# Optimization experiments

Hardware: AMD Instinct MI355X
Metric: run time of the kernel (lower is better)

Reference implementation:

```python
import jax, jax.numpy as jnp
import numpy as np

CHUNK = 256  # rows of z processed per scan step; keeps [CHUNK, M, D] intermediate ~64MB


def setup_inputs() -> dict:
    key = jax.random.key(0)
    k1, k2, k3, k4 = jax.random.split(key, 4)
    N, M, D = 2048, 512, 128
    z = jax.random.normal(k1, (N, D), dtype=jnp.float32)
    e = jax.random.normal(k2, (M, D), dtype=jnp.float32)
    probs = jax.random.uniform(k3, (N,), dtype=jnp.float32)
    dropout = jax.random.uniform(k4, (N, D), dtype=jnp.float32)
    return {"z": z, "e": e, "probs": probs, "dropout": dropout}


def reference(z, e, probs, dropout):
    # z: [N, D], e: [M, D]
    N, D = z.shape
    M = e.shape[0]
    nchunk = N // CHUNK

    def body(carry, zc):
        # zc: [CHUNK, D]
        min_sum, min_elem = carry  # [M], [M, D]
        # elementwise squared differences for this chunk: [CHUNK, M, D]
        delem = (zc[:, None, :] - e[None, :, :]) ** 2
        dsum = jnp.sum(delem, axis=2)                      # [CHUNK, M]
        min_sum = jnp.minimum(min_sum, jnp.min(dsum, axis=0))
        min_elem = jnp.minimum(min_elem, jnp.min(delem, axis=0))
        return (min_sum, min_elem), None

    init = (jnp.full((M,), jnp.inf, dtype=z.dtype),
            jnp.full((M, D), jnp.inf, dtype=z.dtype))
    (min_sum, min_elem), _ = jax.lax.scan(body, init, z.reshape(nchunk, CHUNK, D))

    # torch: mean over M of min over N of sum_d distance
    min_loss = jnp.mean(min_sum)
    # torch: mean over (M, D) of elementwise min over N
    wise_min_loss = jnp.mean(min_elem)

    # z = z * (dropout < probs[:, None])  -- boolean mask multiply
    z_out = z * (dropout < probs[:, None]).astype(z.dtype)
    return min_loss, wise_min_loss, z_out
```

## Files before the change

### kernel.cpp

```cpp
#include <hip/hip_runtime.h>


#define N_ 2048
#define M_ 512
#define D_ 128
#define ME_OFF  M_
#define CNT_OFF (M_ + M_ * D_)
#define POISON  0xAAAAAAAAu
#define CONTRIB 768u

__global__ void __launch_bounds__(256, 2) k_all(
        const float* __restrict__ z, const float* __restrict__ e,
        const float* __restrict__ probs, const float* __restrict__ drop,
        float* __restrict__ out, unsigned int* __restrict__ ws) {
    const int bx = blockIdx.x;
    const int t  = threadIdx.x;
    bool contrib = true;

    if (bx < 512) {
        const int mg = bx >> 3, chunk = bx & 7;
        const int d = t & 127, half = t >> 7;
        const int m0 = mg * 8 + half * 4;
        const int n0 = chunk * 256;

        const float e0 = e[(m0 + 0) * D_ + d];
        const float e1 = e[(m0 + 1) * D_ + d];
        const float e2 = e[(m0 + 2) * D_ + d];
        const float e3 = e[(m0 + 3) * D_ + d];

        float me0 = __uint_as_float(0x7f800000u), me1 = me0, me2 = me0, me3 = me0;
        const float* zp = z + n0 * D_ + d;
        #pragma unroll 8
        for (int i = 0; i < 256; ++i) {
            float zv = zp[i * D_];
            float df;
            df = zv - e0; me0 = fminf(me0, df * df);
            df = zv - e1; me1 = fminf(me1, df * df);
            df = zv - e2; me2 = fminf(me2, df * df);
            df = zv - e3; me3 = fminf(me3, df * df);
        }
        unsigned int* me = ws + ME_OFF + m0 * D_ + d;
        atomicMin(me + 0 * D_, __float_as_uint(me0));
        atomicMin(me + 1 * D_, __float_as_uint(me1));
        atomicMin(me + 2 * D_, __float_as_uint(me2));
        atomicMin(me + 3 * D_, __float_as_uint(me3));
    } else if (bx < 768) {
        const int b = bx - 512;
        const int nb = b >> 5, mt = b & 31;
        const int n = nb * 256 + t;
        const int m0 = mt * 16;

        float4 zr[32];
        const float4* z4 = reinterpret_cast<const float4*>(z) + n * 32;
        #pragma unroll
        for (int j = 0; j < 32; ++j) zr[j] = z4[j];

        const float4* e4 = reinterpret_cast<const float4*>(e);
        for (int mi = 0; mi < 16; mi += 2) {
            const int ma = m0 + mi;
            const int mb = ma + 1;
            float a0 = 0.f, a1 = 0.f, a2 = 0.f, a3 = 0.f;
            float b0 = 0.f, b1 = 0.f, b2 = 0.f, b3 = 0.f;
            #pragma unroll
            for (int j = 0; j < 32; ++j) {
                float4 ea = e4[ma * 32 + j];
                float4 eb = e4[mb * 32 + j];
                float dx, dy, dz, dw;
                dx = zr[j].x - ea.x; a0 = fmaf(dx, dx, a0);
                dy = zr[j].y - ea.y; a1 = fmaf(dy, dy, a1);
                dz = zr[j].z - ea.z; a2 = fmaf(dz, dz, a2);
                dw = zr[j].w - ea.w; a3 = fmaf(dw, dw, a3);
                dx = zr[j].x - eb.x; b0 = fmaf(dx, dx, b0);
                dy = zr[j].y - eb.y; b1 = fmaf(dy, dy, b1);
                dz = zr[j].z - eb.z; b2 = fmaf(dz, dz, b2);
                dw = zr[j].w - eb.w; b3 = fmaf(dw, dw, b3);
            }
            float sa = (a0 + a1) + (a2 + a3);
            float sb = (b0 + b1) + (b2 + b3);
            #pragma unroll
            for (int off = 32; off; off >>= 1) {
                sa = fminf(sa, __shfl_xor(sa, off));
                sb = fminf(sb, __shfl_xor(sb, off));
            }
            if ((t & 63) == 0) {
                atomicMin(&ws[ma], __float_as_uint(sa));
                atomicMin(&ws[mb], __float_as_uint(sb));
            }
        }
    } else {
        contrib = false;
        const int b = bx - 768;
        const int i = b * 256 + t;
        const int n = i >> 5;
        const float p = probs[n];
        const float4 zv = reinterpret_cast<const float4*>(z)[i];
        const float4 dv = reinterpret_cast<const float4*>(drop)[i];
        float2 lo, hi;
        lo.x = dv.x < p ? zv.x : 0.f;
        lo.y = dv.y < p ? zv.y : 0.f;
        hi.x = dv.z < p ? zv.z : 0.f;
        hi.y = dv.w < p ? zv.w : 0.f;
        float2* o = reinterpret_cast<float2*>(out + 2) + i * 2;
        o[0] = lo;
        o[1] = hi;
    }

    if (!contrib) return;

    __shared__ unsigned int lastFlag;
    __syncthreads();
    if (t == 0) {
        __threadfence();
        unsigned int old = atomicAdd(ws + CNT_OFF, 1u);
        lastFlag = (old == POISON + (CONTRIB - 1u)) | (old == CONTRIB - 1u);
    }
    __syncthreads();
    if (!lastFlag) return;

    __threadfence();
    const float* wf = reinterpret_cast<const float*>(ws);

    float s_elem = 0.f;
    const float4* me4 = reinterpret_cast<const float4*>(wf + ME_OFF);
    #pragma unroll 8
    for (int k = 0; k < 64; ++k) {
        float4 v = me4[k * 256 + t];
        s_elem += (v.x + v.y) + (v.z + v.w);
    }
    float s_sum = 0.f;
    if (t < 128) {
        float4 u = reinterpret_cast<const float4*>(wf)[t];
        s_sum = (u.x + u.y) + (u.z + u.w);
    }
    #pragma unroll
    for (int off = 32; off; off >>= 1) {
        s_elem += __shfl_xor(s_elem, off);
        s_sum  += __shfl_xor(s_sum, off);
    }
    __shared__ float sm[8];
    const int w = t >> 6;
    if ((t & 63) == 0) { sm[w] = s_elem; sm[4 + w] = s_sum; }
    __syncthreads();
    if (t == 0) {
        float te = sm[0] + sm[1] + sm[2] + sm[3];
        float ts = sm[4] + sm[5] + sm[6] + sm[7];
        out[0] = ts * (1.0f / 512.0f);
        out[1] = te * (1.0f / 65536.0f);
    }
}

extern "C" void kernel_launch(void* const* d_in, const int* in_sizes, int n_in,
                              void* d_out, int out_size, void* d_ws, size_t ws_size,
                              hipStream_t stream) {
    const float* z     = (const float*)d_in[0];
    const float* e     = (const float*)d_in[1];
    const float* probs = (const float*)d_in[2];
    const float* drop  = (const float*)d_in[3];
    float* out = (float*)d_out;
    unsigned int* ws = (unsigned int*)d_ws;

    k_all<<<dim3(1024), dim3(256), 0, stream>>>(z, e, probs, drop, out, ws);
}
```

Measured before the change: 100.1 us.

## Restructure distance-sum blocks to stream z and keep sixteen accumulators

The sum-distance branch no longer holds a whole z row (32 float4) in registers. It streams z one float4 at a time and updates 16 running sums, one per codebook row, so each z load is reused across 16 rows and the shuffle reductions and atomics are batched. Launch bounds are raised to 4 blocks per SM and the elementwise-min loop unroll is doubled. This lowers register pressure to raise occupancy, at the cost of a single serial FMA chain per accumulator and more e loads per z element.

```diff
diff --git a/kernel.cpp b/kernel.cpp
--- a/kernel.cpp
+++ b/kernel.cpp
@@ -9,7 +9,7 @@
 #define POISON  0xAAAAAAAAu
 #define CONTRIB 768u
 
-__global__ void __launch_bounds__(256, 2) k_all(
+__global__ void __launch_bounds__(256, 4) k_all(
         const float* __restrict__ z, const float* __restrict__ e,
         const float* __restrict__ probs, const float* __restrict__ drop,
         float* __restrict__ out, unsigned int* __restrict__ ws) {
@@ -30,7 +30,7 @@
 
         float me0 = __uint_as_float(0x7f800000u), me1 = me0, me2 = me0, me3 = me0;
         const float* zp = z + n0 * D_ + d;
-        #pragma unroll 8
+        #pragma unroll 16
         for (int i = 0; i < 256; ++i) {
             float zv = zp[i * D_];
             float df;
@@ -50,42 +50,35 @@
         const int n = nb * 256 + t;
         const int m0 = mt * 16;
 
-        float4 zr[32];
+        float s[16];
+        #pragma unroll
+        for (int k = 0; k < 16; ++k) s[k] = 0.f;
+
         const float4* z4 = reinterpret_cast<const float4*>(z) + n * 32;
+        const float4* e4 = reinterpret_cast<const float4*>(e) + m0 * 32;
+
+        #pragma unroll 4
+        for (int j = 0; j < 32; ++j) {
+            const float4 zv = z4[j];
+            #pragma unroll
+            for (int k = 0; k < 16; ++k) {
+                const float4 ev = e4[k * 32 + j];
+                float dx = zv.x - ev.x; s[k] = fmaf(dx, dx, s[k]);
+                float dy = zv.y - ev.y; s[k] = fmaf(dy, dy, s[k]);
+                float dz = zv.z - ev.z; s[k] = fmaf(dz, dz, s[k]);
+                float dw = zv.w - ev.w; s[k] = fmaf(dw, dw, s[k]);
+            }
+        }
         #pragma unroll
-        for (int j = 0; j < 32; ++j) zr[j] = z4[j];
-
-        const float4* e4 = reinterpret_cast<const float4*>(e);
-        for (int mi = 0; mi < 16; mi += 2) {
-            const int ma = m0 + mi;
-            const int mb = ma + 1;
-            float a0 = 0.f, a1 = 0.f, a2 = 0.f, a3 = 0.f;
-            float b0 = 0.f, b1 = 0.f, b2 = 0.f, b3 = 0.f;
+        for (int off = 32; off; off >>= 1) {
             #pragma unroll
-            for (int j = 0; j < 32; ++j) {
-                float4 ea = e4[ma * 32 + j];
-                float4 eb = e4[mb * 32 + j];
-                float dx, dy, dz, dw;
-                dx = zr[j].x - ea.x; a0 = fmaf(dx, dx, a0);
-                dy = zr[j].y - ea.y; a1 = fmaf(dy, dy, a1);
-                dz = zr[j].z - ea.z; a2 = fmaf(dz, dz, a2);
-                dw = zr[j].w - ea.w; a3 = fmaf(dw, dw, a3);
-                dx = zr[j].x - eb.x; b0 = fmaf(dx, dx, b0);
-                dy = zr[j].y - eb.y; b1 = fmaf(dy, dy, b1);
-                dz = zr[j].z - eb.z; b2 = fmaf(dz, dz, b2);
-                dw = zr[j].w - eb.w; b3 = fmaf(dw, dw, b3);
-            }
-            float sa = (a0 + a1) + (a2 + a3);
-            float sb = (b0 + b1) + (b2 + b3);
+            for (int k = 0; k < 16; ++k)
+                s[k] = fminf(s[k], __shfl_xor(s[k], off));
+        }
+        if ((t & 63) == 0) {
             #pragma unroll
-            for (int off = 32; off; off >>= 1) {
-                sa = fminf(sa, __shfl_xor(sa, off));
-                sb = fminf(sb, __shfl_xor(sb, off));
-            }
-            if ((t & 63) == 0) {
-                atomicMin(&ws[ma], __float_as_uint(sa));
-                atomicMin(&ws[mb], __float_as_uint(sb));
-            }
+            for (int k = 0; k < 16; ++k)
+                atomicMin(&ws[m0 + k], __float_as_uint(s[k]));
         }
     } else {
         contrib = false;
```

New measurement: 120.5 us. 1.2x slower.
